# Performance work log

Measured on AMD Instinct MI355X. Metric: run time of the kernel, lower is better.

The kernel has to match this reference:

```python
import jax, jax.numpy as jnp
import numpy as np

N, IN_DIM, HID, HEADS, HOPS, NCLS, E = 20000, 1536, 256, 4, 3, 3, 320000
HD = HID // HEADS
EPS = 1e-5
NEG_SLOPE = 0.2


def layer_norm(x, g, b):
    mu = jnp.mean(x, axis=-1, keepdims=True)
    var = jnp.var(x, axis=-1, keepdims=True)
    return (x - mu) * jax.lax.rsqrt(var + EPS) * g + b


def gatv2(x, src, dst, Wl, bl, Wr, br, att, bias):
    # x: [N, HID]; src/dst: [E'] (self loops included)
    xl = (x @ Wl + bl).reshape(N, HEADS, HD)  # source transform
    xr = (x @ Wr + br).reshape(N, HEADS, HD)  # target transform
    e = jax.nn.leaky_relu(xl[src] + xr[dst], NEG_SLOPE)          # [E', H, D]
    logits = jnp.einsum('ehd,hd->eh', e, att)                     # [E', H]
    m = jax.ops.segment_max(logits, dst, num_segments=N)         # [N, H]
    ex = jnp.exp(logits - m[dst])
    denom = jax.ops.segment_sum(ex, dst, num_segments=N)
    alpha = ex / denom[dst]                                       # softmax per dst
    msg = xl[src] * alpha[:, :, None]                             # [E', H, D]
    out = jax.ops.segment_sum(msg, dst, num_segments=N)
    return out.reshape(N, HID) + bias


def setup_inputs() -> dict:
    key = jax.random.key(0)
    ks = jax.random.split(key, 20)
    s = lambda k, shp, sc: jax.random.normal(k, shp, jnp.float32) * sc
    return {
        'features': s(ks[0], (N, IN_DIM), 1.0),
        'edge_index': jax.random.randint(ks[1], (2, E), 0, N, jnp.int64),
        'proj_W': s(ks[2], (IN_DIM, HID), 0.02),
        'proj_b': jnp.zeros((HID,), jnp.float32),
        'n0_g': jnp.ones((HID,), jnp.float32),
        'n0_b': jnp.zeros((HID,), jnp.float32),
        'Wl': s(ks[3], (HOPS, HID, HID), 0.05),
        'bl': jnp.zeros((HOPS, HID), jnp.float32),
        'Wr': s(ks[4], (HOPS, HID, HID), 0.05),
        'br': jnp.zeros((HOPS, HID), jnp.float32),
        'att': s(ks[5], (HOPS, HEADS, HD), 0.1),
        'gbias': jnp.zeros((HOPS, HID), jnp.float32),
        'ln_g': jnp.ones((HOPS, HID), jnp.float32),
        'ln_b': jnp.zeros((HOPS, HID), jnp.float32),
        'h1_W': s(ks[6], (HID, HID), 0.05),
        'h1_b': jnp.zeros((HID,), jnp.float32),
        'h2_W': s(ks[7], (HID, NCLS), 0.05),
        'h2_b': jnp.zeros((NCLS,), jnp.float32),
    }


def reference(features, edge_index, proj_W, proj_b, n0_g, n0_b, Wl, bl, Wr, br,
              att, gbias, ln_g, ln_b, h1_W, h1_b, h2_W, h2_b):
    # add self loops (PyG GATv2Conv default)
    loop = jnp.arange(N, dtype=edge_index.dtype)
    src = jnp.concatenate([edge_index[0], loop])
    dst = jnp.concatenate([edge_index[1], loop])

    x = layer_norm(features @ proj_W + proj_b, n0_g, n0_b)
    for h in range(HOPS):
        g = gatv2(x, src, dst, Wl[h], bl[h], Wr[h], br[h], att[h], gbias[h])
        x = layer_norm(g + x, ln_g[h], ln_b[h])
    # head (dropout inactive at eval); torch GELU is exact erf form
    x = jax.nn.gelu(x @ h1_W + h1_b, approximate=False)
    return x @ h2_W + h2_b
```

## Files before the change

kernel.cpp:

```cpp
#include <hip/hip_runtime.h>
#include <hip/hip_bf16.h>
#include <math.h>

#define NN 20000
#define MPAD 20096
#define INDIM 1536
#define HID 256
#define NE 320000
#define NEDGE (NE + NN)
#define EPSV 1e-5f
#define NEG 0.2f

typedef unsigned short ushort_b;
typedef unsigned int uint32;
typedef __bf16 bf16x8 __attribute__((ext_vector_type(8)));
typedef float f32x4 __attribute__((ext_vector_type(4)));

#define AS1(p) ((const __attribute__((address_space(1))) void*)(p))
#define AS3(p) ((__attribute__((address_space(3))) void*)(p))

__device__ inline ushort_b f2bf(float x) {
  union { float f; uint32 u; } v; v.f = x;
  uint32 r = v.u + 0x7FFFu + ((v.u >> 16) & 1u);
  return (ushort_b)(r >> 16);
}
__device__ inline float bf2f(ushort_b h) {
  union { uint32 u; float f; } v; v.u = ((uint32)h) << 16;
  return v.f;
}
__device__ inline float4 ldbf4(const ushort_b* p) {
  ushort4 u = *(const ushort4*)p;
  float4 f;
  f.x = bf2f(u.x); f.y = bf2f(u.y); f.z = bf2f(u.z); f.w = bf2f(u.w);
  return f;
}

template<int AFP32, int OUTMODE>
__global__ __launch_bounds__(256) void gemm_mfma(
    const void* __restrict__ Av,
    const ushort_b* __restrict__ Bt0, const ushort_b* __restrict__ Bt1,
    const float* __restrict__ bias0, const float* __restrict__ bias1,
    void* __restrict__ C0, void* __restrict__ C1,
    int Mstore, int Kloop, int Kstride, int kb0, int kb1)
{
  __shared__ ushort_b As0[64 * 32], As1[64 * 32];
  __shared__ ushort_b Bs0[128 * 32], Bs1[128 * 32];
  const ushort_b* Bt = blockIdx.z ? Bt1 : Bt0;
  const float* bias  = blockIdx.z ? bias1 : bias0;
  void* Cv           = blockIdx.z ? C1 : C0;
  int kbase          = blockIdx.z ? kb1 : kb0;

  int tid = threadIdx.x;
  int wave = tid >> 6, lane = tid & 63;
  int r0 = blockIdx.y * 64;
  int c0 = blockIdx.x * 128;
  int wn = wave << 5;
  int mrow = lane & 15, quad = lane >> 4;
  int nk = Kloop >> 5;

  const float* Af = (const float*)Av;
  const ushort_b* Ab = (const ushort_b*)Av;

  f32x4 acc[4][2] = {};
  float4 pA0[2], pA1[2];

  auto issueB = [&](int k0, ushort_b* lds) {
#pragma unroll
    for (int it = 0; it < 2; it++) {
      int off = (wave << 10) + (it << 12) + (lane << 4);
      int row = off >> 6, colb = off & 63;
      const char* g = (const char*)Bt + ((size_t)(c0 + row) * Kstride + kbase + k0) * 2 + colb;
      __builtin_amdgcn_global_load_lds(AS1(g), AS3((char*)lds + off), 16, 0, 0);
    }
  };
  auto issueA = [&](int k0, ushort_b* lds) {
    int off = tid << 4;
    int row = off >> 6, colb = off & 63;
    const char* g = (const char*)Ab + ((size_t)(r0 + row) * Kstride + kbase + k0) * 2 + colb;
    __builtin_amdgcn_global_load_lds(AS1(g), AS3((char*)lds + off), 16, 0, 0);
  };
  auto loadA = [&](int k0, float4* dst) {
#pragma unroll
    for (int p = 0; p < 2; p++) {
      int off4 = (p << 8) + tid;
      int row = off4 >> 3, col4 = off4 & 7;
      int grow = r0 + row;
      dst[p] = (grow < Mstore)
          ? *(const float4*)(Af + (size_t)grow * Kstride + kbase + k0 + (col4 << 2))
          : make_float4(0.f, 0.f, 0.f, 0.f);
    }
  };
  auto writeA = [&](const float4* src, ushort_b* lds) {
#pragma unroll
    for (int p = 0; p < 2; p++) {
      int off4 = (p << 8) + tid;
      int row = off4 >> 3, col4 = off4 & 7;
      uint2 u;
      u.x = (uint32)f2bf(src[p].x) | ((uint32)f2bf(src[p].y) << 16);
      u.y = (uint32)f2bf(src[p].z) | ((uint32)f2bf(src[p].w) << 16);
      *(uint2*)(lds + (row << 5) + (col4 << 2)) = u;
    }
  };
  auto computeStage = [&](const ushort_b* Asb, const ushort_b* Bsb) {
    bf16x8 af[4], bfr[2];
#pragma unroll
    for (int t = 0; t < 4; t++)
      af[t] = *(const bf16x8*)(Asb + (((t << 4) + mrow) << 5) + (quad << 3));
#pragma unroll
    for (int u = 0; u < 2; u++)
      bfr[u] = *(const bf16x8*)(Bsb + ((wn + (u << 4) + mrow) << 5) + (quad << 3));
#pragma unroll
    for (int t = 0; t < 4; t++)
#pragma unroll
      for (int u = 0; u < 2; u++)
        acc[t][u] = __builtin_amdgcn_mfma_f32_16x16x32_bf16(af[t], bfr[u], acc[t][u], 0, 0, 0);
  };

  if (AFP32) {
    loadA(0, pA0);
    issueB(0, Bs0);
    loadA(32, pA1);
    writeA(pA0, As0);
  } else {
    issueA(0, As0);
    issueB(0, Bs0);
  }

  for (int k = 0; k < nk; k += 2) {
    __syncthreads();
    if (k + 1 < nk) {
      issueB((k + 1) << 5, Bs1);
      if (AFP32) {
        writeA(pA1, As1);
        if (k + 2 < nk) loadA((k + 2) << 5, pA0);
      } else {
        issueA((k + 1) << 5, As1);
      }
    }
    computeStage(As0, Bs0);
    __syncthreads();
    if (k + 2 < nk) {
      issueB((k + 2) << 5, Bs0);
      if (AFP32) {
        writeA(pA0, As0);
        if (k + 3 < nk) loadA((k + 3) << 5, pA1);
      } else {
        issueA((k + 2) << 5, As0);
      }
    }
    computeStage(As1, Bs1);
  }

#pragma unroll
  for (int u = 0; u < 2; u++) {
    int col = c0 + wn + (u << 4) + mrow;
    float bb = bias[col];
#pragma unroll
    for (int t = 0; t < 4; t++) {
#pragma unroll
      for (int r = 0; r < 4; r++) {
        int row = r0 + (t << 4) + (quad << 2) + r;
        if (row < Mstore) {
          float v = acc[t][u][r] + bb;
          if (OUTMODE == 3) v = 0.5f * v * (1.f + erff(v * 0.70710678118654752f));
          if (OUTMODE == 0) ((float*)Cv)[(size_t)row * 256 + col] = v;
          else              ((ushort_b*)Cv)[(size_t)row * 256 + col] = f2bf(v);
        }
      }
    }
  }
}

__global__ __launch_bounds__(256) void transpose_cast(
    const float* __restrict__ in, ushort_b* __restrict__ out, int R, int C)
{
  __shared__ float t[32][33];
  int bx = blockIdx.x * 32;
  int by = blockIdx.y * 32;
  for (int i = threadIdx.y; i < 32; i += 8)
    t[i][threadIdx.x] = in[(size_t)(by + i) * C + bx + threadIdx.x];
  __syncthreads();
  for (int i = threadIdx.y; i < 32; i += 8)
    out[(size_t)(bx + i) * R + by + threadIdx.x] = f2bf(t[threadIdx.x][i]);
}

__global__ __launch_bounds__(256) void transpose7(
    const float* __restrict__ Wl, const float* __restrict__ Wr,
    const float* __restrict__ h1W, ushort_b* __restrict__ dst_base)
{
  int z = blockIdx.z;
  const float* in = (z < 3) ? Wl + (size_t)z * 65536
                  : (z < 6) ? Wr + (size_t)(z - 3) * 65536
                            : h1W;
  ushort_b* out = dst_base + (size_t)z * 65536;
  __shared__ float t[32][33];
  int bx = blockIdx.x * 32;
  int by = blockIdx.y * 32;
  for (int i = threadIdx.y; i < 32; i += 8)
    t[i][threadIdx.x] = in[(size_t)(by + i) * 256 + bx + threadIdx.x];
  __syncthreads();
  for (int i = threadIdx.y; i < 32; i += 8)
    out[(size_t)(bx + i) * 256 + by + threadIdx.x] = f2bf(t[threadIdx.x][i]);
}

__global__ __launch_bounds__(256) void ln_sum_kernel(
    const float* __restrict__ in0, const float* __restrict__ in1,
    const float* __restrict__ g, const float* __restrict__ b,
    float* __restrict__ out, ushort_b* __restrict__ bf_out, int n)
{
  int wave = threadIdx.x >> 6, lane = threadIdx.x & 63;
  int row = blockIdx.x * 4 + wave;
  if (row >= n) return;
  int c = lane << 2;
  float4 v = *(const float4*)(in0 + (size_t)row * HID + c);
  float4 v1 = *(const float4*)(in1 + (size_t)row * HID + c);
  v.x += v1.x; v.y += v1.y; v.z += v1.z; v.w += v1.w;
  float s1 = v.x + v.y + v.z + v.w;
  float s2 = v.x * v.x + v.y * v.y + v.z * v.z + v.w * v.w;
#pragma unroll
  for (int m = 1; m < 64; m <<= 1) {
    s1 += __shfl_xor(s1, m, 64);
    s2 += __shfl_xor(s2, m, 64);
  }
  float mu = s1 * (1.f / 256.f);
  float var = s2 * (1.f / 256.f) - mu * mu;
  float rstd = rsqrtf(var + EPSV);
  float4 gv = *(const float4*)(g + c);
  float4 bv = *(const float4*)(b + c);
  float4 o;
  o.x = (v.x - mu) * rstd * gv.x + bv.x;
  o.y = (v.y - mu) * rstd * gv.y + bv.y;
  o.z = (v.z - mu) * rstd * gv.z + bv.z;
  o.w = (v.w - mu) * rstd * gv.w + bv.w;
  *(float4*)(out + (size_t)row * HID + c) = o;
  ushort4 ub;
  ub.x = f2bf(o.x); ub.y = f2bf(o.y); ub.z = f2bf(o.z); ub.w = f2bf(o.w);
  *(ushort4*)(bf_out + (size_t)row * HID + c) = ub;
}

__global__ void count_kernel(const int* __restrict__ ei, int* __restrict__ cnt)
{
  int e = blockIdx.x * blockDim.x + threadIdx.x;
  if (e < NEDGE) {
    int d = (e < NE) ? ei[NE + e] : (e - NE);
    atomicAdd(&cnt[d], 1);
  }
}

__global__ __launch_bounds__(1024) void scan_kernel(
    const int* __restrict__ cnt, int* __restrict__ offs, int* __restrict__ cursor)
{
  __shared__ int sums[1024];
  int tid = threadIdx.x;
  const int CH = 20;
  int base = tid * CH;
  int loc[CH];
  int s = 0;
#pragma unroll
  for (int i = 0; i < CH; i++) {
    int idx = base + i;
    int v = (idx < NN) ? cnt[idx] : 0;
    loc[i] = s;
    s += v;
  }
  sums[tid] = s;
  __syncthreads();
  for (int off = 1; off < 1024; off <<= 1) {
    int t = (tid >= off) ? sums[tid - off] : 0;
    __syncthreads();
    sums[tid] += t;
    __syncthreads();
  }
  int pre = (tid == 0) ? 0 : sums[tid - 1];
#pragma unroll
  for (int i = 0; i < CH; i++) {
    int idx = base + i;
    if (idx < NN) { int e = pre + loc[i]; offs[idx] = e; cursor[idx] = e; }
  }
  if (tid == 0) offs[NN] = NEDGE;
}

__global__ void scatter_kernel(const int* __restrict__ ei, int* __restrict__ cursor,
                               int* __restrict__ csr_src)
{
  int e = blockIdx.x * blockDim.x + threadIdx.x;
  if (e < NEDGE) {
    int s, d;
    if (e < NE) { s = ei[e]; d = ei[NE + e]; }
    else { s = e - NE; d = e - NE; }
    int p = atomicAdd(&cursor[d], 1);
    csr_src[p] = s;
  }
}

__device__ inline float edge_logit(float4 xv, float4 xrv, float4 attv) {
  float e0 = xv.x + xrv.x, e1 = xv.y + xrv.y, e2 = xv.z + xrv.z, e3 = xv.w + xrv.w;
  e0 = (e0 > 0.f) ? e0 : NEG * e0;
  e1 = (e1 > 0.f) ? e1 : NEG * e1;
  e2 = (e2 > 0.f) ? e2 : NEG * e2;
  e3 = (e3 > 0.f) ? e3 : NEG * e3;
  float lc = e0 * attv.x + e1 * attv.y + e2 * attv.z + e3 * attv.w;
  lc += __shfl_xor(lc, 1, 16);
  lc += __shfl_xor(lc, 2, 16);
  lc += __shfl_xor(lc, 4, 16);
  lc += __shfl_xor(lc, 8, 16);
  return lc;
}

#define ACCUM(i, lg, xv) {                          \
    float w = __expf(lg);                            \
    lS[i] += w;                                      \
    pS##i##0 += w * xv.x; pS##i##1 += w * xv.y;      \
    pS##i##2 += w * xv.z; pS##i##3 += w * xv.w; }

__global__ __launch_bounds__(256) void gat_kernel(
    const ushort_b* __restrict__ xl, const ushort_b* __restrict__ xr,
    const float* __restrict__ x_in, const float* __restrict__ att,
    const float* __restrict__ gbias, const float* __restrict__ ln_g,
    const float* __restrict__ ln_b, const int* __restrict__ offs,
    const int* __restrict__ csr_src, float* __restrict__ x_out,
    ushort_b* __restrict__ xb_out)
{
  __shared__ float gbuf[2][64][5];
  int wave = threadIdx.x >> 6, lane = threadIdx.x & 63;
  int nib = wave >> 1, sub = wave & 1;
  int node = blockIdx.x * 2 + nib;
  int c = lane << 2;
  float4 xrv = ldbf4(xr + (size_t)node * HID + c);
  float4 attv = *(const float4*)(att + c);

  float lS[4] = {0.f, 0.f, 0.f, 0.f};
  float pS00 = 0.f, pS01 = 0.f, pS02 = 0.f, pS03 = 0.f;
  float pS10 = 0.f, pS11 = 0.f, pS12 = 0.f, pS13 = 0.f;
  float pS20 = 0.f, pS21 = 0.f, pS22 = 0.f, pS23 = 0.f;
  float pS30 = 0.f, pS31 = 0.f, pS32 = 0.f, pS33 = 0.f;

  int beg = offs[node], end = offs[node + 1];
  int mid = beg + ((end - beg + 1) >> 1);
  int e  = sub ? mid : beg;
  int e1 = sub ? end : mid;
  for (; e + 3 < e1; e += 4) {
    int s0 = csr_src[e], s1 = csr_src[e + 1], s2 = csr_src[e + 2], s3 = csr_src[e + 3];
    float4 x0v = ldbf4(xl + (size_t)s0 * HID + c);
    float4 x1v = ldbf4(xl + (size_t)s1 * HID + c);
    float4 x2v = ldbf4(xl + (size_t)s2 * HID + c);
    float4 x3v = ldbf4(xl + (size_t)s3 * HID + c);
    float g0 = edge_logit(x0v, xrv, attv);
    float g1 = edge_logit(x1v, xrv, attv);
    float g2 = edge_logit(x2v, xrv, attv);
    float g3 = edge_logit(x3v, xrv, attv);
    ACCUM(0, g0, x0v);
    ACCUM(1, g1, x1v);
    ACCUM(2, g2, x2v);
    ACCUM(3, g3, x3v);
  }
  for (; e < e1; e++) {
    int s0 = csr_src[e];
    float4 x0v = ldbf4(xl + (size_t)s0 * HID + c);
    float g0 = edge_logit(x0v, xrv, attv);
    ACCUM(0, g0, x0v);
  }

  float l  = lS[0] + lS[1] + lS[2] + lS[3];
  float q0 = pS00 + pS10 + pS20 + pS30;
  float q1 = pS01 + pS11 + pS21 + pS31;
  float q2 = pS02 + pS12 + pS22 + pS32;
  float q3 = pS03 + pS13 + pS23 + pS33;

  if (sub) {
    gbuf[nib][lane][0] = l;
    gbuf[nib][lane][1] = q0;
    gbuf[nib][lane][2] = q1;
    gbuf[nib][lane][3] = q2;
    gbuf[nib][lane][4] = q3;
  }
  __syncthreads();
  if (sub) return;

  l  += gbuf[nib][lane][0];
  q0 += gbuf[nib][lane][1];
  q1 += gbuf[nib][lane][2];
  q2 += gbuf[nib][lane][3];
  q3 += gbuf[nib][lane][4];

  float inv = 1.f / l;
  float4 xv = *(const float4*)(x_in + (size_t)node * HID + c);
  float4 gb = *(const float4*)(gbias + c);
  float o0 = q0 * inv + gb.x + xv.x;
  float o1 = q1 * inv + gb.y + xv.y;
  float o2 = q2 * inv + gb.z + xv.z;
  float o3 = q3 * inv + gb.w + xv.w;
  float s1s = o0 + o1 + o2 + o3;
  float s2s = o0 * o0 + o1 * o1 + o2 * o2 + o3 * o3;
#pragma unroll
  for (int mmk = 1; mmk < 64; mmk <<= 1) {
    s1s += __shfl_xor(s1s, mmk, 64);
    s2s += __shfl_xor(s2s, mmk, 64);
  }
  float mu = s1s * (1.f / 256.f);
  float var = s2s * (1.f / 256.f) - mu * mu;
  float rstd = rsqrtf(var + EPSV);
  float4 gv = *(const float4*)(ln_g + c);
  float4 bv = *(const float4*)(ln_b + c);
  float4 o;
  o.x = (o0 - mu) * rstd * gv.x + bv.x;
  o.y = (o1 - mu) * rstd * gv.y + bv.y;
  o.z = (o2 - mu) * rstd * gv.z + bv.z;
  o.w = (o3 - mu) * rstd * gv.w + bv.w;
  *(float4*)(x_out + (size_t)node * HID + c) = o;
  ushort4 ub;
  ub.x = f2bf(o.x); ub.y = f2bf(o.y); ub.z = f2bf(o.z); ub.w = f2bf(o.w);
  *(ushort4*)(xb_out + (size_t)node * HID + c) = ub;
}

__global__ __launch_bounds__(256) void head2_kernel(
    const ushort_b* __restrict__ t1, const float* __restrict__ W,
    const float* __restrict__ bias, float* __restrict__ out)
{
  int wave = threadIdx.x >> 6, lane = threadIdx.x & 63;
  int row = blockIdx.x * 4 + wave;
  if (row >= NN) return;
  int c = lane << 2;
  float4 v = ldbf4(t1 + (size_t)row * HID + c);
  float p0 = 0.f, p1 = 0.f, p2 = 0.f;
#pragma unroll
  for (int j = 0; j < 4; j++) {
    float vj = (&v.x)[j];
    p0 += vj * W[(c + j) * 3 + 0];
    p1 += vj * W[(c + j) * 3 + 1];
    p2 += vj * W[(c + j) * 3 + 2];
  }
#pragma unroll
  for (int mm = 1; mm < 64; mm <<= 1) {
    p0 += __shfl_xor(p0, mm, 64);
    p1 += __shfl_xor(p1, mm, 64);
    p2 += __shfl_xor(p2, mm, 64);
  }
  if (lane == 0) {
    out[(size_t)row * 3 + 0] = p0 + bias[0];
    out[(size_t)row * 3 + 1] = p1 + bias[1];
    out[(size_t)row * 3 + 2] = p2 + bias[2];
  }
}

extern "C" void kernel_launch(void* const* d_in, const int* in_sizes, int n_in,
                              void* d_out, int out_size, void* d_ws, size_t ws_size,
                              hipStream_t stream)
{
  const float* features = (const float*)d_in[0];
  const int*   ei       = (const int*)d_in[1];
  const float* proj_W   = (const float*)d_in[2];
  const float* proj_b   = (const float*)d_in[3];
  const float* n0_g     = (const float*)d_in[4];
  const float* n0_b     = (const float*)d_in[5];
  const float* Wl       = (const float*)d_in[6];
  const float* bl       = (const float*)d_in[7];
  const float* Wr       = (const float*)d_in[8];
  const float* br       = (const float*)d_in[9];
  const float* att      = (const float*)d_in[10];
  const float* gbias    = (const float*)d_in[11];
  const float* ln_g     = (const float*)d_in[12];
  const float* ln_b     = (const float*)d_in[13];
  const float* h1_W     = (const float*)d_in[14];
  const float* h1_b     = (const float*)d_in[15];
  const float* h2_W     = (const float*)d_in[16];
  const float* h2_b     = (const float*)d_in[17];
  float* out = (float*)d_out;

  char* w = (char*)d_ws;
  float*    x0    = (float*)w;    w += (size_t)NN * HID * 4;
  float*    x1    = (float*)w;    w += (size_t)NN * HID * 4;
  float*    part1 = (float*)w;    w += (size_t)NN * HID * 4;
  ushort_b* xlb   = (ushort_b*)w; w += (size_t)NN * HID * 2;
  ushort_b* xrb   = (ushort_b*)w; w += (size_t)NN * HID * 2;
  ushort_b* xb    = (ushort_b*)w; w += (size_t)MPAD * HID * 2;
  ushort_b* wtp   = (ushort_b*)w; w += (size_t)HID * INDIM * 2;
  ushort_b* wtl   = (ushort_b*)w; w += (size_t)3 * HID * HID * 2;
  ushort_b* wtr   = (ushort_b*)w; w += (size_t)3 * HID * HID * 2;
  ushort_b* wth1  = (ushort_b*)w; w += (size_t)HID * HID * 2;
  float* zbias = (float*)w; w += (size_t)HID * 4;
  int* cnt     = (int*)w;  w += (size_t)NN * 4;
  int* offs    = (int*)w;  w += (size_t)(NN + 1) * 4;
  int* cursor  = (int*)w;  w += (size_t)NN * 4;
  int* csr     = (int*)w;  w += (size_t)NEDGE * 4;

  hipMemsetAsync(cnt, 0, (size_t)NN * 4, stream);
  hipMemsetAsync(zbias, 0, (size_t)HID * 4, stream);
  hipMemsetAsync(xb + (size_t)NN * HID, 0, (size_t)(MPAD - NN) * HID * 2, stream);
  count_kernel<<<(NEDGE + 255) / 256, 256, 0, stream>>>(ei, cnt);
  scan_kernel<<<1, 1024, 0, stream>>>(cnt, offs, cursor);
  scatter_kernel<<<(NEDGE + 255) / 256, 256, 0, stream>>>(ei, cursor, csr);

  transpose_cast<<<dim3(HID / 32, INDIM / 32), dim3(32, 8), 0, stream>>>(proj_W, wtp, INDIM, HID);
  transpose7<<<dim3(8, 8, 7), dim3(32, 8), 0, stream>>>(Wl, Wr, h1_W, wtl);

  dim3 gsplit(2, MPAD / 64, 2);
  dim3 gsingle(2, MPAD / 64, 1);

  gemm_mfma<1, 0><<<gsplit, 256, 0, stream>>>(
      features, wtp, wtp, proj_b, zbias, x1, part1, NN, INDIM / 2, INDIM, 0, INDIM / 2);
  ln_sum_kernel<<<(NN + 3) / 4, 256, 0, stream>>>(x1, part1, n0_g, n0_b, x0, xb, NN);

  float* xcur = x0;
  float* xnxt = x1;
  for (int h = 0; h < 3; h++) {
    gemm_mfma<0, 2><<<gsplit, 256, 0, stream>>>(
        xb, wtl + (size_t)h * HID * HID, wtr + (size_t)h * HID * HID,
        bl + h * HID, br + h * HID, xlb, xrb, NN, HID, HID, 0, 0);
    gat_kernel<<<NN / 2, 256, 0, stream>>>(
        xlb, xrb, xcur, att + h * HID, gbias + h * HID,
        ln_g + h * HID, ln_b + h * HID, offs, csr, xnxt, xb);
    float* t = xcur; xcur = xnxt; xnxt = t;
  }

  gemm_mfma<0, 3><<<gsingle, 256, 0, stream>>>(
      xb, wth1, wth1, h1_b, h1_b, xlb, xlb, NN, HID, HID, 0, 0);
  head2_kernel<<<(NN + 3) / 4, 256, 0, stream>>>(xlb, h2_W, h2_b, out);
}
```

Measured before the change: 560.1 us.

## Enlarge GEMM tiles to 128x128, use 4-way split-K projection, fuse transposes

The MFMA GEMM moves from a 64x128 block tile to 128x128, with each wave computing a 64x64 sub-tile (4x4 MFMAs per k-step) for more operand reuse out of LDS. The input projection switches from 2-way to 4-way split-K, writing partials into consecutive workspace buffers. A new LayerNorm kernel sums the four partials and also zero-fills the padded bf16 rows, which removes two memsets and the zero-bias buffer. All weight transposes now run in a single launch. In exchange, each wave holds more accumulator registers, so occupancy may drop, and the hop GEMMs get half as many row blocks.

Result: no change. 570.9 us (+1.9%).

```diff
diff --git a/kernel.cpp b/kernel.cpp
--- a/kernel.cpp
+++ b/kernel.cpp
@@ -35,34 +35,45 @@
   return f;
 }
 
-template<int AFP32, int OUTMODE>
+template<int AFP32, int OUTMODE, int SPLITK>
 __global__ __launch_bounds__(256) void gemm_mfma(
     const void* __restrict__ Av,
     const ushort_b* __restrict__ Bt0, const ushort_b* __restrict__ Bt1,
     const float* __restrict__ bias0, const float* __restrict__ bias1,
     void* __restrict__ C0, void* __restrict__ C1,
-    int Mstore, int Kloop, int Kstride, int kb0, int kb1)
-{
-  __shared__ ushort_b As0[64 * 32], As1[64 * 32];
+    int Mstore, int Kloop, int Kstride)
+{
+  __shared__ ushort_b As0[128 * 32], As1[128 * 32];
   __shared__ ushort_b Bs0[128 * 32], Bs1[128 * 32];
-  const ushort_b* Bt = blockIdx.z ? Bt1 : Bt0;
-  const float* bias  = blockIdx.z ? bias1 : bias0;
-  void* Cv           = blockIdx.z ? C1 : C0;
-  int kbase          = blockIdx.z ? kb1 : kb0;
+  const ushort_b* Bt;
+  const float* bias;
+  void* Cv;
+  int kbase;
+  if (SPLITK > 1) {
+    Bt = Bt0;
+    bias = (blockIdx.z == 0) ? bias0 : nullptr;
+    Cv = (float*)C0 + (size_t)blockIdx.z * NN * HID;
+    kbase = blockIdx.z * Kloop;
+  } else {
+    Bt = blockIdx.z ? Bt1 : Bt0;
+    bias = blockIdx.z ? bias1 : bias0;
+    Cv = blockIdx.z ? C1 : C0;
+    kbase = 0;
+  }
 
   int tid = threadIdx.x;
   int wave = tid >> 6, lane = tid & 63;
-  int r0 = blockIdx.y * 64;
+  int r0 = blockIdx.y * 128;
   int c0 = blockIdx.x * 128;
-  int wn = wave << 5;
+  int wm = (wave >> 1) << 6, wn = (wave & 1) << 6;
   int mrow = lane & 15, quad = lane >> 4;
   int nk = Kloop >> 5;
 
   const float* Af = (const float*)Av;
   const ushort_b* Ab = (const ushort_b*)Av;
 
-  f32x4 acc[4][2] = {};
-  float4 pA0[2], pA1[2];
+  f32x4 acc[4][4] = {};
+  float4 pA0[4], pA1[4];
 
   auto issueB = [&](int k0, ushort_b* lds) {
 #pragma unroll
@@ -74,14 +85,17 @@
     }
   };
   auto issueA = [&](int k0, ushort_b* lds) {
-    int off = tid << 4;
-    int row = off >> 6, colb = off & 63;
-    const char* g = (const char*)Ab + ((size_t)(r0 + row) * Kstride + kbase + k0) * 2 + colb;
-    __builtin_amdgcn_global_load_lds(AS1(g), AS3((char*)lds + off), 16, 0, 0);
+#pragma unroll
+    for (int it = 0; it < 2; it++) {
+      int off = (wave << 10) + (it << 12) + (lane << 4);
+      int row = off >> 6, colb = off & 63;
+      const char* g = (const char*)Ab + ((size_t)(r0 + row) * Kstride + kbase + k0) * 2 + colb;
+      __builtin_amdgcn_global_load_lds(AS1(g), AS3((char*)lds + off), 16, 0, 0);
+    }
   };
   auto loadA = [&](int k0, float4* dst) {
 #pragma unroll
-    for (int p = 0; p < 2; p++) {
+    for (int p = 0; p < 4; p++) {
       int off4 = (p << 8) + tid;
       int row = off4 >> 3, col4 = off4 & 7;
       int grow = r0 + row;
@@ -92,7 +106,7 @@
   };
   auto writeA = [&](const float4* src, ushort_b* lds) {
 #pragma unroll
-    for (int p = 0; p < 2; p++) {
+    for (int p = 0; p < 4; p++) {
       int off4 = (p << 8) + tid;
       int row = off4 >> 3, col4 = off4 & 7;
       uint2 u;
@@ -102,18 +116,17 @@
     }
   };
   auto computeStage = [&](const ushort_b* Asb, const ushort_b* Bsb) {
-    bf16x8 af[4], bfr[2];
-#pragma unroll
-    for (int t = 0; t < 4; t++)
-      af[t] = *(const bf16x8*)(Asb + (((t << 4) + mrow) << 5) + (quad << 3));
-#pragma unroll
-    for (int u = 0; u < 2; u++)
-      bfr[u] = *(const bf16x8*)(Bsb + ((wn + (u << 4) + mrow) << 5) + (quad << 3));
-#pragma unroll
-    for (int t = 0; t < 4; t++)
-#pragma unroll
-      for (int u = 0; u < 2; u++)
-        acc[t][u] = __builtin_amdgcn_mfma_f32_16x16x32_bf16(af[t], bfr[u], acc[t][u], 0, 0, 0);
+    bf16x8 af[4], bfr[4];
+#pragma unroll
+    for (int t = 0; t < 4; t++) {
+      af[t]  = *(const bf16x8*)(Asb + ((wm + (t << 4) + mrow) << 5) + (quad << 3));
+      bfr[t] = *(const bf16x8*)(Bsb + ((wn + (t << 4) + mrow) << 5) + (quad << 3));
+    }
+#pragma unroll
+    for (int mt = 0; mt < 4; mt++)
+#pragma unroll
+      for (int nt = 0; nt < 4; nt++)
+        acc[mt][nt] = __builtin_amdgcn_mfma_f32_16x16x32_bf16(af[mt], bfr[nt], acc[mt][nt], 0, 0, 0);
   };
 
   if (AFP32) {
@@ -152,16 +165,16 @@
   }
 
 #pragma unroll
-  for (int u = 0; u < 2; u++) {
-    int col = c0 + wn + (u << 4) + mrow;
-    float bb = bias[col];
-#pragma unroll
-    for (int t = 0; t < 4; t++) {
+  for (int nt = 0; nt < 4; nt++) {
+    int col = c0 + wn + (nt << 4) + mrow;
+    float bb = bias ? bias[col] : 0.f;
+#pragma unroll
+    for (int mt = 0; mt < 4; mt++) {
 #pragma unroll
       for (int r = 0; r < 4; r++) {
-        int row = r0 + (t << 4) + (quad << 2) + r;
+        int row = r0 + wm + (mt << 4) + (quad << 2) + r;
         if (row < Mstore) {
-          float v = acc[t][u][r] + bb;
+          float v = acc[mt][nt][r] + bb;
           if (OUTMODE == 3) v = 0.5f * v * (1.f + erff(v * 0.70710678118654752f));
           if (OUTMODE == 0) ((float*)Cv)[(size_t)row * 256 + col] = v;
           else              ((ushort_b*)Cv)[(size_t)row * 256 + col] = f2bf(v);
@@ -171,50 +184,55 @@
   }
 }
 
-__global__ __launch_bounds__(256) void transpose_cast(
-    const float* __restrict__ in, ushort_b* __restrict__ out, int R, int C)
+__global__ __launch_bounds__(256) void transpose_all(
+    const float* __restrict__ Wl, const float* __restrict__ Wr,
+    const float* __restrict__ h1W, const float* __restrict__ projW,
+    ushort_b* __restrict__ wbase, ushort_b* __restrict__ wtp)
 {
   __shared__ float t[32][33];
-  int bx = blockIdx.x * 32;
-  int by = blockIdx.y * 32;
-  for (int i = threadIdx.y; i < 32; i += 8)
-    t[i][threadIdx.x] = in[(size_t)(by + i) * C + bx + threadIdx.x];
-  __syncthreads();
-  for (int i = threadIdx.y; i < 32; i += 8)
-    out[(size_t)(bx + i) * R + by + threadIdx.x] = f2bf(t[threadIdx.x][i]);
-}
-
-__global__ __launch_bounds__(256) void transpose7(
-    const float* __restrict__ Wl, const float* __restrict__ Wr,
-    const float* __restrict__ h1W, ushort_b* __restrict__ dst_base)
-{
   int z = blockIdx.z;
-  const float* in = (z < 3) ? Wl + (size_t)z * 65536
-                  : (z < 6) ? Wr + (size_t)(z - 3) * 65536
-                            : h1W;
-  ushort_b* out = dst_base + (size_t)z * 65536;
-  __shared__ float t[32][33];
-  int bx = blockIdx.x * 32;
-  int by = blockIdx.y * 32;
-  for (int i = threadIdx.y; i < 32; i += 8)
-    t[i][threadIdx.x] = in[(size_t)(by + i) * 256 + bx + threadIdx.x];
-  __syncthreads();
-  for (int i = threadIdx.y; i < 32; i += 8)
-    out[(size_t)(bx + i) * 256 + by + threadIdx.x] = f2bf(t[threadIdx.x][i]);
-}
-
-__global__ __launch_bounds__(256) void ln_sum_kernel(
-    const float* __restrict__ in0, const float* __restrict__ in1,
-    const float* __restrict__ g, const float* __restrict__ b,
-    float* __restrict__ out, ushort_b* __restrict__ bf_out, int n)
+  int tx = threadIdx.x;
+  if (z < 7) {
+    const float* in = (z < 3) ? Wl + (size_t)z * 65536
+                    : (z < 6) ? Wr + (size_t)(z - 3) * 65536
+                              : h1W;
+    ushort_b* out = wbase + (size_t)z * 65536;
+    int bx = blockIdx.x * 32, by = blockIdx.y * 32;
+    for (int i = threadIdx.y; i < 32; i += 8)
+      t[i][tx] = in[(size_t)(by + i) * 256 + bx + tx];
+    __syncthreads();
+    for (int i = threadIdx.y; i < 32; i += 8)
+      out[(size_t)(bx + i) * 256 + by + tx] = f2bf(t[tx][i]);
+  } else {
+    if (blockIdx.y) return;
+    int by = (z - 7) * 32;
+    int bx = blockIdx.x * 32;
+    for (int i = threadIdx.y; i < 32; i += 8)
+      t[i][tx] = projW[(size_t)(by + i) * 256 + bx + tx];
+    __syncthreads();
+    for (int i = threadIdx.y; i < 32; i += 8)
+      wtp[(size_t)(bx + i) * INDIM + by + tx] = f2bf(t[tx][i]);
+  }
+}
+
+__global__ __launch_bounds__(256) void ln_sum4_kernel(
+    const float* __restrict__ parts, const float* __restrict__ g,
+    const float* __restrict__ b, float* __restrict__ out,
+    ushort_b* __restrict__ bf_out)
 {
   int wave = threadIdx.x >> 6, lane = threadIdx.x & 63;
   int row = blockIdx.x * 4 + wave;
-  if (row >= n) return;
   int c = lane << 2;
-  float4 v = *(const float4*)(in0 + (size_t)row * HID + c);
-  float4 v1 = *(const float4*)(in1 + (size_t)row * HID + c);
-  v.x += v1.x; v.y += v1.y; v.z += v1.z; v.w += v1.w;
+  if (row >= NN) {
+    if (row < MPAD) *(ushort4*)(bf_out + (size_t)row * HID + c) = make_ushort4(0, 0, 0, 0);
+    return;
+  }
+  float4 v = *(const float4*)(parts + (size_t)row * HID + c);
+#pragma unroll
+  for (int k = 1; k < 4; k++) {
+    float4 p = *(const float4*)(parts + (size_t)k * NN * HID + (size_t)row * HID + c);
+    v.x += p.x; v.y += p.y; v.z += p.z; v.w += p.w;
+  }
   float s1 = v.x + v.y + v.z + v.w;
   float s2 = v.x * v.x + v.y * v.y + v.z * v.z + v.w * v.w;
 #pragma unroll
@@ -478,42 +496,40 @@
   ushort_b* wtl   = (ushort_b*)w; w += (size_t)3 * HID * HID * 2;
   ushort_b* wtr   = (ushort_b*)w; w += (size_t)3 * HID * HID * 2;
   ushort_b* wth1  = (ushort_b*)w; w += (size_t)HID * HID * 2;
-  float* zbias = (float*)w; w += (size_t)HID * 4;
   int* cnt     = (int*)w;  w += (size_t)NN * 4;
   int* offs    = (int*)w;  w += (size_t)(NN + 1) * 4;
   int* cursor  = (int*)w;  w += (size_t)NN * 4;
   int* csr     = (int*)w;  w += (size_t)NEDGE * 4;
+  (void)part1;
 
   hipMemsetAsync(cnt, 0, (size_t)NN * 4, stream);
-  hipMemsetAsync(zbias, 0, (size_t)HID * 4, stream);
-  hipMemsetAsync(xb + (size_t)NN * HID, 0, (size_t)(MPAD - NN) * HID * 2, stream);
   count_kernel<<<(NEDGE + 255) / 256, 256, 0, stream>>>(ei, cnt);
   scan_kernel<<<1, 1024, 0, stream>>>(cnt, offs, cursor);
   scatter_kernel<<<(NEDGE + 255) / 256, 256, 0, stream>>>(ei, cursor, csr);
 
-  transpose_cast<<<dim3(HID / 32, INDIM / 32), dim3(32, 8), 0, stream>>>(proj_W, wtp, INDIM, HID);
-  transpose7<<<dim3(8, 8, 7), dim3(32, 8), 0, stream>>>(Wl, Wr, h1_W, wtl);
-
-  dim3 gsplit(2, MPAD / 64, 2);
-  dim3 gsingle(2, MPAD / 64, 1);
-
-  gemm_mfma<1, 0><<<gsplit, 256, 0, stream>>>(
-      features, wtp, wtp, proj_b, zbias, x1, part1, NN, INDIM / 2, INDIM, 0, INDIM / 2);
-  ln_sum_kernel<<<(NN + 3) / 4, 256, 0, stream>>>(x1, part1, n0_g, n0_b, x0, xb, NN);
+  transpose_all<<<dim3(8, 8, 55), dim3(32, 8), 0, stream>>>(Wl, Wr, h1_W, proj_W, wtl, wtp);
+
+  dim3 gproj(2, MPAD / 128, 4);
+  dim3 ghop(2, MPAD / 128, 2);
+  dim3 gone(2, MPAD / 128, 1);
+
+  gemm_mfma<1, 0, 4><<<gproj, 256, 0, stream>>>(
+      features, wtp, nullptr, proj_b, nullptr, x0, nullptr, NN, INDIM / 4, INDIM);
+  ln_sum4_kernel<<<MPAD / 4, 256, 0, stream>>>(x0, n0_g, n0_b, x0, xb);
 
   float* xcur = x0;
   float* xnxt = x1;
   for (int h = 0; h < 3; h++) {
-    gemm_mfma<0, 2><<<gsplit, 256, 0, stream>>>(
+    gemm_mfma<0, 2, 1><<<ghop, 256, 0, stream>>>(
         xb, wtl + (size_t)h * HID * HID, wtr + (size_t)h * HID * HID,
-        bl + h * HID, br + h * HID, xlb, xrb, NN, HID, HID, 0, 0);
+        bl + h * HID, br + h * HID, xlb, xrb, NN, HID, HID);
     gat_kernel<<<NN / 2, 256, 0, stream>>>(
         xlb, xrb, xcur, att + h * HID, gbias + h * HID,
         ln_g + h * HID, ln_b + h * HID, offs, csr, xnxt, xb);
     float* t = xcur; xcur = xnxt; xnxt = t;
   }
 
-  gemm_mfma<0, 3><<<gsingle, 256, 0, stream>>>(
-      xb, wth1, wth1, h1_b, h1_b, xlb, xlb, NN, HID, HID, 0, 0);
+  gemm_mfma<0, 3, 1><<<gone, 256, 0, stream>>>(
+      xb, wth1, wth1, h1_b, h1_b, xlb, xlb, NN, HID, HID);
   head2_kernel<<<(NN + 3) / 4, 256, 0, stream>>>(xlb, h2_W, h2_b, out);
 }
```
